# Optimization experiments

Measured on AMD Instinct MI355X. Metric: run time of the kernel, lower is better.

Reference implementation:

```python
import jax, jax.numpy as jnp
import numpy as np

B, S, HID, MEM, NW = 32, 256, 1024, 256, 1024
PLAST, IMP = 0.1, 1.0
W_SCALE = 0.02  # sane init for projection weights


def setup_inputs() -> dict:
    key = jax.random.key(0)
    ks = jax.random.split(key, 24)
    n = lambda k, sh, s=1.0: jax.random.normal(k, sh, dtype=jnp.float32) * s
    inp = {
        "q": n(ks[0], (B, S, HID)),
        "data": n(ks[1], (NW, HID)),
        "episodic_k": n(ks[2], (MEM, HID)),
        "episodic_v": n(ks[3], (MEM, HID)),
        "semantic_k": n(ks[4], (MEM, HID)),
        "semantic_v": n(ks[5], (MEM, HID)),
        "working_m": n(ks[6], (1, 10, HID)),
    }
    i = 7
    for name in ("atte", "atts", "attw"):
        inp[name + "_in_w"] = n(ks[i], (3 * HID, HID), W_SCALE); i += 1
        inp[name + "_in_b"] = jnp.zeros((3 * HID,), jnp.float32)
        inp[name + "_out_w"] = n(ks[i], (HID, HID), W_SCALE); i += 1
        inp[name + "_out_b"] = jnp.zeros((HID,), jnp.float32)
    inp["proj_w"] = n(ks[i], (HID, 3 * HID), W_SCALE)
    inp["proj_b"] = jnp.zeros((HID,), jnp.float32)
    return inp


def mha_shared_kv(q, k, v, in_w, in_b, out_w, out_b, n_heads):
    # q: [B,S,H]; k,v: [M,H] (memory bank shared across the batch)
    d = q.shape[-1] // n_heads
    wq, wk, wv = jnp.split(in_w, 3, axis=0)
    bq, bk, bv = jnp.split(in_b, 3)
    Bq, Sq, _ = q.shape
    M = k.shape[0]
    qh = (q @ wq.T + bq).reshape(Bq, Sq, n_heads, d)   # [B,S,h,d]
    kh = (k @ wk.T + bk).reshape(M, n_heads, d)        # [M,h,d]
    vh = (v @ wv.T + bv).reshape(M, n_heads, d)
    scale = 1.0 / jnp.sqrt(jnp.float32(d))
    att = jax.nn.softmax(jnp.einsum('bshd,mhd->bhsm', qh, kh) * scale, axis=-1)
    o = jnp.einsum('bhsm,mhd->bshd', att, vh).reshape(Bq, Sq, -1)
    return o @ out_w.T + out_b


def reference(q, data, episodic_k, episodic_v, semantic_k, semantic_v, working_m,
              atte_in_w, atte_in_b, atte_out_w, atte_out_b,
              atts_in_w, atts_in_b, atts_out_w, atts_out_b,
              attw_in_w, attw_in_b, attw_out_w, attw_out_b,
              proj_w, proj_b):
    # ---- write(data, 'episodic'): softmax-addressed fast-weight update ----
    probs = jax.nn.softmax(data @ episodic_k.T, axis=-1)          # [N,M]
    w = probs * (PLAST * IMP)                                     # [N,M]
    u = w.mean(axis=0)[:, None]                                   # [M,1] mean update strength per slot
    writes = jnp.einsum('nm,nh->mh', w, data) / NW                # mean_n data[n]*w[n,m]
    ek = jax.lax.stop_gradient(episodic_k * (1.0 - u) + writes)   # .data assignment -> no grad
    ev = jax.lax.stop_gradient(episodic_v * (1.0 - u) + writes)
    # ---- read(q): 3 small attentions over memory banks, concat, project ----
    e_r = mha_shared_kv(q, ek, ev, atte_in_w, atte_in_b, atte_out_w, atte_out_b, 16)
    s_r = mha_shared_kv(q, semantic_k, semantic_v, atts_in_w, atts_in_b, atts_out_w, atts_out_b, 16)
    w_r = mha_shared_kv(q, working_m[0], working_m[0], attw_in_w, attw_in_b, attw_out_w, attw_out_b, 8)
    cat = jnp.concatenate((e_r, s_r, w_r), axis=-1)               # [B,S,3H]
    return cat @ proj_w.T + proj_b                                # [B,S,H]
```

## Files before the change

### kernel.cpp

```cpp
#include <hip/hip_runtime.h>
#include <hip/hip_bf16.h>


using bf = __hip_bfloat16;
using short8v = __attribute__((ext_vector_type(8))) short;
using f32x4  = __attribute__((ext_vector_type(4))) float;

#define GLOAD_LDS16(g, l) __builtin_amdgcn_global_load_lds( \
    (const __attribute__((address_space(1))) void*)(g), \
    (__attribute__((address_space(3))) void*)(l), 16, 0, 0)

__device__ inline float bf2f(unsigned short s) {
    union { unsigned u; float f; } c; c.u = ((unsigned)s) << 16; return c.f;
}
__device__ inline unsigned short f2bu(float x) {
    union { float f; unsigned u; } c; c.f = x;
    unsigned r = c.u + 0x7FFF + ((c.u >> 16) & 1);
    return (unsigned short)(r >> 16);
}
__device__ inline void storeC(float* p, float v) { *p = v; }
__device__ inline void storeC(bf* p, float v) { *p = __float2bfloat16(v); }

__global__ __launch_bounds__(256) void gemm_bt(
    const bf* __restrict__ A, int lda,
    const bf* __restrict__ B, int ldb,
    float* __restrict__ part, int M, int N, int K)
{
    __shared__ short As[128 * 64];
    __shared__ short Bs[128 * 64];
    const int nbn = N >> 7;
    const int bm = blockIdx.x / nbn, bn = blockIdx.x % nbn;
    const int t = threadIdx.x;
    const int w = t >> 6, lane = t & 63;
    const int wr = w >> 1, wc = w & 1;
    const int l16 = lane & 15, lhi = lane >> 4;
    const int kc = K / gridDim.y;
    const int kbeg = blockIdx.y * kc, kend = kbeg + kc;

    f32x4 acc[4][4];
    #pragma unroll
    for (int i = 0; i < 4; ++i)
        #pragma unroll
        for (int j = 0; j < 4; ++j) { f32x4 z = {0.f, 0.f, 0.f, 0.f}; acc[i][j] = z; }

    const bf* Arow = A + (size_t)bm * 128 * lda;
    const bf* Brow = B + (size_t)bn * 128 * ldb;

    for (int k0 = kbeg; k0 < kend; k0 += 64) {
        #pragma unroll
        for (int j = 0; j < 4; ++j) {
            int u = (w * 4 + j) * 64 + lane;
            int row = u >> 3, c8 = u & 7;
            int slot = c8 ^ (row & 7);
            GLOAD_LDS16(Brow + (size_t)row * ldb + k0 + slot * 8, &Bs[(w * 4 + j) * 512]);
            GLOAD_LDS16(Arow + (size_t)row * lda + k0 + slot * 8, &As[(w * 4 + j) * 512]);
        }
        __syncthreads();
        #pragma unroll
        for (int kk = 0; kk < 2; ++kk) {
            short8v af[4], bfr[4];
            #pragma unroll
            for (int mt = 0; mt < 4; ++mt) {
                int row = wr * 64 + mt * 16 + l16;
                int slot = (kk * 4 + lhi) ^ (row & 7);
                af[mt] = *(const short8v*)&As[row * 64 + slot * 8];
            }
            #pragma unroll
            for (int nt = 0; nt < 4; ++nt) {
                int row = wc * 64 + nt * 16 + l16;
                int slot = (kk * 4 + lhi) ^ (row & 7);
                bfr[nt] = *(const short8v*)&Bs[row * 64 + slot * 8];
            }
            #pragma unroll
            for (int mt = 0; mt < 4; ++mt)
                #pragma unroll
                for (int nt = 0; nt < 4; ++nt)
                    acc[mt][nt] = __builtin_amdgcn_mfma_f32_16x16x32_bf16(
                        af[mt], bfr[nt], acc[mt][nt], 0, 0, 0);
        }
        __syncthreads();
    }
    #pragma unroll
    for (int mt = 0; mt < 4; ++mt)
        #pragma unroll
        for (int nt = 0; nt < 4; ++nt) {
            int col = bn * 128 + wc * 64 + nt * 16 + l16;
            #pragma unroll
            for (int j = 0; j < 4; ++j) {
                int rowg = bm * 128 + wr * 64 + mt * 16 + lhi * 4 + j;
                part[(size_t)blockIdx.y * M * N + (size_t)rowg * N + col] = acc[mt][nt][j];
            }
        }
}

template <typename CT>
__global__ __launch_bounds__(512) void gemm256(
    const bf* __restrict__ A, int lda,
    const bf* __restrict__ B, int ldb,
    const float* __restrict__ bias,
    CT* __restrict__ C, int ldc,
    int M, int N, int K)
{
    __shared__ short As[256 * 64];
    __shared__ short Bs[128 * 64];
    const int nbn = N >> 7;
    int bid = blockIdx.x;
    bid = (bid & 7) * (gridDim.x >> 3) + (bid >> 3);
    const int bm = bid / nbn, bn = bid % nbn;
    const int t = threadIdx.x;
    const int w = t >> 6, lane = t & 63;
    const int wr = w >> 1, wc = w & 1;
    const int l16 = lane & 15, lhi = lane >> 4;

    f32x4 acc[4][4];
    #pragma unroll
    for (int i = 0; i < 4; ++i)
        #pragma unroll
        for (int j = 0; j < 4; ++j) { f32x4 z = {0.f, 0.f, 0.f, 0.f}; acc[i][j] = z; }

    const bf* Arow = A + (size_t)bm * 256 * lda;
    const bf* Brow = B + (size_t)bn * 128 * ldb;

    for (int k0 = 0; k0 < K; k0 += 64) {
        #pragma unroll
        for (int j = 0; j < 2; ++j) {
            int u = t + (j << 9);
            int row = u >> 3, c8 = u & 7;
            int slot = c8 ^ (row & 7);
            GLOAD_LDS16(Brow + (size_t)row * ldb + k0 + slot * 8, &Bs[(j * 8 + w) * 512]);
        }
        #pragma unroll
        for (int j = 0; j < 4; ++j) {
            int u = t + (j << 9);
            int row = u >> 3, c8 = u & 7;
            int slot = c8 ^ (row & 7);
            GLOAD_LDS16(Arow + (size_t)row * lda + k0 + slot * 8, &As[(j * 8 + w) * 512]);
        }
        __syncthreads();
        #pragma unroll
        for (int kk = 0; kk < 2; ++kk) {
            short8v af[4], bfr[4];
            #pragma unroll
            for (int mt = 0; mt < 4; ++mt) {
                int row = wr * 64 + mt * 16 + l16;
                int slot = (kk * 4 + lhi) ^ (row & 7);
                af[mt] = *(const short8v*)&As[row * 64 + slot * 8];
            }
            #pragma unroll
            for (int nt = 0; nt < 4; ++nt) {
                int row = wc * 64 + nt * 16 + l16;
                int slot = (kk * 4 + lhi) ^ (row & 7);
                bfr[nt] = *(const short8v*)&Bs[row * 64 + slot * 8];
            }
            #pragma unroll
            for (int mt = 0; mt < 4; ++mt)
                #pragma unroll
                for (int nt = 0; nt < 4; ++nt)
                    acc[mt][nt] = __builtin_amdgcn_mfma_f32_16x16x32_bf16(
                        af[mt], bfr[nt], acc[mt][nt], 0, 0, 0);
        }
        __syncthreads();
    }
    #pragma unroll
    for (int mt = 0; mt < 4; ++mt)
        #pragma unroll
        for (int nt = 0; nt < 4; ++nt) {
            int col = bn * 128 + wc * 64 + nt * 16 + l16;
            float bv = bias ? bias[col] : 0.0f;
            #pragma unroll
            for (int j = 0; j < 4; ++j) {
                int rowg = bm * 256 + wr * 64 + mt * 16 + lhi * 4 + j;
                storeC(&C[(size_t)rowg * ldc + col], acc[mt][nt][j] + bv);
            }
        }
}

template <typename CT>
__global__ __launch_bounds__(512) void gemm256db(
    const bf* __restrict__ A, int lda,
    const bf* __restrict__ B, int ldb,
    const float* __restrict__ bias,
    CT* __restrict__ C, int ldc,
    int M, int N, int K)
{
    __shared__ short As0[256 * 64];
    __shared__ short Bs0[128 * 64];
    __shared__ short As1[256 * 64];
    __shared__ short Bs1[128 * 64];
    const int nbn = N >> 7;
    int bid = blockIdx.x;
    bid = (bid & 7) * (gridDim.x >> 3) + (bid >> 3);
    const int bm = bid / nbn, bn = bid % nbn;
    const int t = threadIdx.x;
    const int w = t >> 6, lane = t & 63;
    const int wr = w >> 1, wc = w & 1;
    const int l16 = lane & 15, lhi = lane >> 4;

    f32x4 acc[4][4];
    #pragma unroll
    for (int i = 0; i < 4; ++i)
        #pragma unroll
        for (int j = 0; j < 4; ++j) { f32x4 z = {0.f, 0.f, 0.f, 0.f}; acc[i][j] = z; }

    const bf* Arow = A + (size_t)bm * 256 * lda;
    const bf* Brow = B + (size_t)bn * 128 * ldb;

    auto stage = [&](short* Asd, short* Bsd, int k0) {
        #pragma unroll
        for (int j = 0; j < 2; ++j) {
            int u = t + (j << 9);
            int row = u >> 3, c8 = u & 7;
            int slot = c8 ^ (row & 7);
            GLOAD_LDS16(Brow + (size_t)row * ldb + k0 + slot * 8, &Bsd[(j * 8 + w) * 512]);
        }
        #pragma unroll
        for (int j = 0; j < 4; ++j) {
            int u = t + (j << 9);
            int row = u >> 3, c8 = u & 7;
            int slot = c8 ^ (row & 7);
            GLOAD_LDS16(Arow + (size_t)row * lda + k0 + slot * 8, &Asd[(j * 8 + w) * 512]);
        }
    };
    auto compute = [&](const short* Ass, const short* Bss) {
        #pragma unroll
        for (int kk = 0; kk < 2; ++kk) {
            short8v af[4], bfr[4];
            #pragma unroll
            for (int mt = 0; mt < 4; ++mt) {
                int row = wr * 64 + mt * 16 + l16;
                int slot = (kk * 4 + lhi) ^ (row & 7);
                af[mt] = *(const short8v*)&Ass[row * 64 + slot * 8];
            }
            #pragma unroll
            for (int nt = 0; nt < 4; ++nt) {
                int row = wc * 64 + nt * 16 + l16;
                int slot = (kk * 4 + lhi) ^ (row & 7);
                bfr[nt] = *(const short8v*)&Bss[row * 64 + slot * 8];
            }
            #pragma unroll
            for (int mt = 0; mt < 4; ++mt)
                #pragma unroll
                for (int nt = 0; nt < 4; ++nt)
                    acc[mt][nt] = __builtin_amdgcn_mfma_f32_16x16x32_bf16(
                        af[mt], bfr[nt], acc[mt][nt], 0, 0, 0);
        }
    };

    const int nt_ = K >> 6;
    stage(As0, Bs0, 0);
    stage(As1, Bs1, 64);
    asm volatile("s_waitcnt vmcnt(6)" ::: "memory");
    __builtin_amdgcn_sched_barrier(0);
    __builtin_amdgcn_s_barrier();

    for (int ti = 0; ti < nt_ - 2; ti += 2) {
        compute(As0, Bs0);
        __builtin_amdgcn_s_barrier();
        stage(As0, Bs0, (ti + 2) << 6);
        asm volatile("s_waitcnt vmcnt(6)" ::: "memory");
        __builtin_amdgcn_sched_barrier(0);
        __builtin_amdgcn_s_barrier();
        compute(As1, Bs1);
        __builtin_amdgcn_s_barrier();
        stage(As1, Bs1, (ti + 3) << 6);
        asm volatile("s_waitcnt vmcnt(6)" ::: "memory");
        __builtin_amdgcn_sched_barrier(0);
        __builtin_amdgcn_s_barrier();
    }
    compute(As0, Bs0);
    __builtin_amdgcn_s_barrier();
    asm volatile("s_waitcnt vmcnt(0)" ::: "memory");
    __builtin_amdgcn_sched_barrier(0);
    __builtin_amdgcn_s_barrier();
    compute(As1, Bs1);

    #pragma unroll
    for (int mt = 0; mt < 4; ++mt)
        #pragma unroll
        for (int nt = 0; nt < 4; ++nt) {
            int col = bn * 128 + wc * 64 + nt * 16 + l16;
            float bv = bias ? bias[col] : 0.0f;
            #pragma unroll
            for (int j = 0; j < 4; ++j) {
                int rowg = bm * 256 + wr * 64 + mt * 16 + lhi * 4 + j;
                storeC(&C[(size_t)rowg * ldc + col], acc[mt][nt][j] + bv);
            }
        }
}

struct GG { const bf* A; const bf* B; const float* bias; bf* out;
            int lda, ldb, M, N, ldo, xoff; };
struct GG7 { GG g[7]; };

__global__ __launch_bounds__(256) void ggemm(GG7 P)
{
    __shared__ short As[128 * 64];
    __shared__ short Bs[128 * 64];
    const int bid = blockIdx.x;
    int gidx = 0;
    #pragma unroll
    for (int i = 1; i < 7; ++i) if (bid >= P.g[i].xoff) gidx = i;
    const GG d = P.g[gidx];
    const int lb = bid - d.xoff;
    const int nbn = d.N >> 7;
    const int bm = lb / nbn, bn = lb % nbn;
    const int t = threadIdx.x;
    const int w = t >> 6, lane = t & 63;
    const int wr = w >> 1, wc = w & 1;
    const int l16 = lane & 15, lhi = lane >> 4;

    f32x4 acc[4][4];
    #pragma unroll
    for (int i = 0; i < 4; ++i)
        #pragma unroll
        for (int j = 0; j < 4; ++j) { f32x4 z = {0.f, 0.f, 0.f, 0.f}; acc[i][j] = z; }

    const bf* Afrow = d.A + (size_t)bm * 128 * d.lda;
    const bf* Brow  = d.B + (size_t)bn * 128 * d.ldb;

    for (int k0 = 0; k0 < 1024; k0 += 64) {
        #pragma unroll
        for (int j = 0; j < 4; ++j) {
            int u = (w * 4 + j) * 64 + lane;
            int row = u >> 3, c8 = u & 7;
            int slot = c8 ^ (row & 7);
            GLOAD_LDS16(Brow + (size_t)row * d.ldb + k0 + slot * 8, &Bs[(w * 4 + j) * 512]);
            GLOAD_LDS16(Afrow + (size_t)row * d.lda + k0 + slot * 8, &As[(w * 4 + j) * 512]);
        }
        __syncthreads();
        #pragma unroll
        for (int kk = 0; kk < 2; ++kk) {
            short8v af[4], bfr[4];
            #pragma unroll
            for (int mt = 0; mt < 4; ++mt) {
                int row = wr * 64 + mt * 16 + l16;
                int slot = (kk * 4 + lhi) ^ (row & 7);
                af[mt] = *(const short8v*)&As[row * 64 + slot * 8];
            }
            #pragma unroll
            for (int nt = 0; nt < 4; ++nt) {
                int row = wc * 64 + nt * 16 + l16;
                int slot = (kk * 4 + lhi) ^ (row & 7);
                bfr[nt] = *(const short8v*)&Bs[row * 64 + slot * 8];
            }
            #pragma unroll
            for (int mt = 0; mt < 4; ++mt)
                #pragma unroll
                for (int nt = 0; nt < 4; ++nt)
                    acc[mt][nt] = __builtin_amdgcn_mfma_f32_16x16x32_bf16(
                        af[mt], bfr[nt], acc[mt][nt], 0, 0, 0);
        }
        __syncthreads();
    }
    #pragma unroll
    for (int mt = 0; mt < 4; ++mt)
        #pragma unroll
        for (int nt = 0; nt < 4; ++nt) {
            int col = bn * 128 + wc * 64 + nt * 16 + l16;
            float bv = d.bias ? d.bias[col] : 0.0f;
            #pragma unroll
            for (int j = 0; j < 4; ++j) {
                int rowg = bm * 128 + wr * 64 + mt * 16 + lhi * 4 + j;
                d.out[(size_t)rowg * d.ldo + col]
                    = __float2bfloat16(acc[mt][nt][j] + bv);
            }
        }
}

__global__ __launch_bounds__(512) void attn_es(
    bf* Ocat, const bf* __restrict__ khE, const bf* __restrict__ khS,
    const bf* __restrict__ vTE, const bf* __restrict__ vTS)
{
    __shared__ short Ks[256 * 64];
    __shared__ short Vs[64 * 256];
    const int bank = blockIdx.x >> 10;
    const int lbid = blockIdx.x & 1023;
    const bf* kh  = bank ? khS : khE;
    const bf* vhT = bank ? vTS : vTE;
    bf* QO = Ocat + bank * 1024;
    const int qt = lbid >> 4, head = lbid & 15;
    const int t = threadIdx.x, w = t >> 6, lane = t & 63;
    const int l16 = lane & 15, lhi = lane >> 4;
    const float scale = 0.125f;

    #pragma unroll
    for (int j = 0; j < 4; ++j) {
        int ublk = w * 4 + j;
        int u = ublk * 64 + lane;
        { int row = u >> 3, c8 = u & 7;
          int slot = c8 ^ (row & 7);
          GLOAD_LDS16(kh + (size_t)row * 1024 + head * 64 + slot * 8, &Ks[ublk * 512]); }
        { int row = u >> 5, c16 = u & 31;
          int slot = c16 ^ (row & 7);
          GLOAD_LDS16(vhT + (size_t)(head * 64 + row) * 256 + slot * 8, &Vs[ublk * 512]); }
    }
    const int qr = qt * 128 + w * 16 + l16;
    short8v aq0 = *(const short8v*)(QO + (size_t)qr * 3072 + head * 64 + lhi * 8);
    short8v aq1 = *(const short8v*)(QO + (size_t)qr * 3072 + head * 64 + 32 + lhi * 8);
    __syncthreads();

    f32x4 sc[16];
    #pragma unroll
    for (int nt = 0; nt < 16; ++nt) { f32x4 z = {0.f, 0.f, 0.f, 0.f}; sc[nt] = z; }
    #pragma unroll
    for (int nt = 0; nt < 16; ++nt) {
        int row = nt * 16 + l16;
        #pragma unroll
        for (int kk = 0; kk < 2; ++kk) {
            int slot = (kk * 4 + lhi) ^ (row & 7);
            short8v b = *(const short8v*)&Ks[row * 64 + slot * 8];
            sc[nt] = __builtin_amdgcn_mfma_f32_16x16x32_bf16(kk ? aq1 : aq0, b, sc[nt], 0, 0, 0);
        }
    }
    float inv[4];
    #pragma unroll
    for (int j = 0; j < 4; ++j) {
        float m_ = -1e30f;
        #pragma unroll
        for (int nt = 0; nt < 16; ++nt) m_ = fmaxf(m_, sc[nt][j]);
        #pragma unroll
        for (int off = 8; off; off >>= 1) m_ = fmaxf(m_, __shfl_xor(m_, off));
        float s_ = 0.f;
        #pragma unroll
        for (int nt = 0; nt < 16; ++nt) {
            float e = __expf((sc[nt][j] - m_) * scale);
            sc[nt][j] = e; s_ += e;
        }
        #pragma unroll
        for (int off = 8; off; off >>= 1) s_ += __shfl_xor(s_, off);
        inv[j] = 1.0f / s_;
    }
    __syncthreads();

    char* Pw = (char*)Ks + w * 4096;
    f32x4 oa[4];
    #pragma unroll
    for (int nt = 0; nt < 4; ++nt) { f32x4 z = {0.f, 0.f, 0.f, 0.f}; oa[nt] = z; }
    #pragma unroll
    for (int h = 0; h < 2; ++h) {
        #pragma unroll
        for (int nt = 0; nt < 8; ++nt) {
            int colL = nt * 16 + l16;
            #pragma unroll
            for (int j = 0; j < 4; ++j) {
                int row = lhi * 4 + j;
                *(short*)(Pw + row * 256 + ((colL * 2) ^ ((row & 7) << 4)))
                    = (short)f2bu(sc[h * 8 + nt][j] * inv[j]);
            }
        }
        #pragma unroll
        for (int kk = 0; kk < 4; ++kk) {
            short8v a = *(const short8v*)(Pw + l16 * 256 + (((kk * 32 + lhi * 8) * 2) ^ ((l16 & 7) << 4)));
            #pragma unroll
            for (int nt = 0; nt < 4; ++nt) {
                int row = nt * 16 + l16;
                int m = h * 128 + kk * 32 + lhi * 8;
                short8v b = *(const short8v*)((const char*)Vs + row * 512 + ((m * 2) ^ ((row & 7) << 4)));
                oa[nt] = __builtin_amdgcn_mfma_f32_16x16x32_bf16(a, b, oa[nt], 0, 0, 0);
            }
        }
    }
    #pragma unroll
    for (int nt = 0; nt < 4; ++nt)
        #pragma unroll
        for (int j = 0; j < 4; ++j)
            QO[(size_t)(qt * 128 + w * 16 + lhi * 4 + j) * 3072 + head * 64 + nt * 16 + l16]
                = __float2bfloat16(oa[nt][j]);
}

__global__ __launch_bounds__(256) void attn_w(
    bf* QOp, const bf* __restrict__ khw, const bf* __restrict__ vhw)
{
    const int t = threadIdx.x;
    const int head = t >> 5;
    const int dg = head * 128 + (t & 31) * 4;

    ushort4 kv[10], vv[10];
    #pragma unroll
    for (int m = 0; m < 10; ++m) {
        kv[m] = *(const ushort4*)(khw + (size_t)m * 1024 + dg);
        vv[m] = *(const ushort4*)(vhw + (size_t)m * 1024 + dg);
    }
    #pragma unroll
    for (int r = 0; r < 4; ++r) {
        const int bs = blockIdx.x * 4 + r;
        ushort4 qv = *(const ushort4*)(QOp + (size_t)bs * 3072 + dg);
        float q0 = bf2f(qv.x), q1 = bf2f(qv.y), q2 = bf2f(qv.z), q3 = bf2f(qv.w);
        float s[10];
        #pragma unroll
        for (int m = 0; m < 10; ++m) {
            float pr = q0 * bf2f(kv[m].x) + q1 * bf2f(kv[m].y)
                     + q2 * bf2f(kv[m].z) + q3 * bf2f(kv[m].w);
            #pragma unroll
            for (int off = 16; off; off >>= 1) pr += __shfl_xor(pr, off);
            s[m] = pr * 0.08838834764831845f;
        }
        float mx = s[0];
        #pragma unroll
        for (int m = 1; m < 10; ++m) mx = fmaxf(mx, s[m]);
        float pp[10], sum = 0.f;
        #pragma unroll
        for (int m = 0; m < 10; ++m) { pp[m] = __expf(s[m] - mx); sum += pp[m]; }
        float inv = 1.0f / sum;
        float o0 = 0, o1 = 0, o2 = 0, o3 = 0;
        #pragma unroll
        for (int m = 0; m < 10; ++m) {
            o0 += pp[m] * bf2f(vv[m].x); o1 += pp[m] * bf2f(vv[m].y);
            o2 += pp[m] * bf2f(vv[m].z); o3 += pp[m] * bf2f(vv[m].w);
        }
        bf* op = QOp + (size_t)bs * 3072 + dg;
        op[0] = __float2bfloat16(o0 * inv); op[1] = __float2bfloat16(o1 * inv);
        op[2] = __float2bfloat16(o2 * inv); op[3] = __float2bfloat16(o3 * inv);
    }
}

struct CS { const float* src; bf* dst; int voff; };
struct MP {
    CS cs[13];
    const float* tsrc[4]; bf* tdst[4];
    const float* ow[3]; const float* ob[3]; const float* ib[3];
    float* bp;
    const float* inb_e; const float* inb_s; float* bqcat3;
    const float* wm; const float* inw_w; const float* inb_w;
    bf* khw; bf* vhw;
};

__global__ __launch_bounds__(256) void megaprep(MP P)
{
    __shared__ unsigned short tile[64][65];
    const int bid = blockIdx.x;
    const int t = threadIdx.x;
    if (bid < 20224) {
        int gi = bid * 256 + t;
        int gidx = 0;
        #pragma unroll
        for (int i = 1; i < 13; ++i) if (gi >= P.cs[i].voff) gidx = i;
        int i = (gi - P.cs[gidx].voff) * 4;
        float4 v = *(const float4*)(P.cs[gidx].src + i);
        ushort4 o;
        o.x = f2bu(v.x); o.y = f2bu(v.y); o.z = f2bu(v.z); o.w = f2bu(v.w);
        *(ushort4*)((unsigned short*)P.cs[gidx].dst + i) = o;
    } else if (bid < 21248) {
        int lb = bid - 20224;
        int sel = lb >> 8, bb = lb & 255;
        const float* in = P.tsrc[sel];
        bf* outT = P.tdst[sel];
        int bx = bb & 15, by = bb >> 4;
        int r0 = by * 64, c0 = bx * 64;
        int tr = t >> 4, tc4 = (t & 15) * 4;
        #pragma unroll
        for (int i = 0; i < 4; ++i) {
            int r = tr + i * 16;
            float4 v = *(const float4*)(in + (size_t)(r0 + r) * 1024 + c0 + tc4);
            tile[r][tc4 + 0] = f2bu(v.x); tile[r][tc4 + 1] = f2bu(v.y);
            tile[r][tc4 + 2] = f2bu(v.z); tile[r][tc4 + 3] = f2bu(v.w);
        }
        __syncthreads();
        #pragma unroll
        for (int i = 0; i < 4; ++i) {
            int r = tr + i * 16;
            ushort4 v;
            v.x = tile[tc4 + 0][r]; v.y = tile[tc4 + 1][r];
            v.z = tile[tc4 + 2][r]; v.w = tile[tc4 + 3][r];
            *(ushort4*)((unsigned short*)outT + (size_t)(c0 + r) * 1024 + r0 + tc4) = v;
        }
    } else if (bid < 22016) {
        int g = (bid - 21248) * 4 + (t >> 6);
        int lane = t & 63;
        int bank = g >> 10, j = g & 1023;
        const float* ow = P.ow[bank];
        const float* xx = P.ib[bank] + 2048;
        const float* wrow = ow + (size_t)j * 1024;
        float acc = 0.f;
        #pragma unroll
        for (int cc = 0; cc < 4; ++cc) {
            float4 a = *(const float4*)(wrow + lane * 16 + cc * 4);
            float4 x = *(const float4*)(xx + lane * 16 + cc * 4);
            acc += a.x * x.x + a.y * x.y + a.z * x.z + a.w * x.w;
        }
        #pragma unroll
        for (int off = 32; off; off >>= 1) acc += __shfl_xor(acc, off);
        if (lane == 0) P.bp[g] = acc + P.ob[bank][j];
    } else if (bid < 22028) {
        int i = (bid - 22016) * 256 + t;
        if (i < 1024) P.bqcat3[i] = P.inb_e[i];
        else if (i < 2048) P.bqcat3[i] = P.inb_s[i - 1024];
        else P.bqcat3[i] = P.inb_w[i - 2048];
    } else {
        int o = (bid - 22028) * 4 + (t >> 6);
        int lane = t & 63;
        int sel = o >= 10240;
        int o2 = o - sel * 10240;
        int m = o2 >> 10, c = o2 & 1023;
        const float* wrow = P.inw_w + (size_t)(1024 + sel * 1024 + c) * 1024;
        const float* xrow = P.wm + (size_t)m * 1024;
        float acc = 0.f;
        #pragma unroll
        for (int cc = 0; cc < 4; ++cc) {
            float4 a = *(const float4*)(wrow + lane * 16 + cc * 4);
            float4 x = *(const float4*)(xrow + lane * 16 + cc * 4);
            acc += a.x * x.x + a.y * x.y + a.z * x.z + a.w * x.w;
        }
        #pragma unroll
        for (int off = 32; off; off >>= 1) acc += __shfl_xor(acc, off);
        if (lane == 0) {
            float v = acc + (sel ? 0.f : P.inb_w[1024 + c]);
            (sel ? P.vhw : P.khw)[(size_t)m * 1024 + c] = __float2bfloat16(v);
        }
    }
}


__global__ __launch_bounds__(256) void btot_kern(
    const float* __restrict__ bp, const float* __restrict__ pw,
    const float* __restrict__ pb, float* __restrict__ btot)
{
    int j = blockIdx.x * 4 + (threadIdx.x >> 6);
    int lane = threadIdx.x & 63;
    const float* row = pw + (size_t)j * 3072;
    float acc = 0.f;
    #pragma unroll
    for (int it = 0; it < 12; ++it) {
        int c = lane * 4 + it * 256;
        float4 a = *(const float4*)(row + c);
        float4 x = *(const float4*)(bp + c);
        acc += a.x * x.x + a.y * x.y + a.z * x.z + a.w * x.w;
    }
    #pragma unroll
    for (int off = 32; off; off >>= 1) acc += __shfl_xor(acc, off);
    if (lane == 0) btot[j] = acc + pb[j];
}

__global__ __launch_bounds__(256) void write_softmax_p(const float* __restrict__ part,
                                                       bf* __restrict__ wT)
{
    const int n = blockIdx.x, m = threadIdx.x;
    float s = 0.f;
    #pragma unroll
    for (int k = 0; k < 8; ++k) s += part[(size_t)k * 262144 + n * 256 + m];
    float mx = s;
    #pragma unroll
    for (int off = 32; off; off >>= 1) mx = fmaxf(mx, __shfl_xor(mx, off));
    __shared__ float red[4], red2[4];
    int w = threadIdx.x >> 6;
    if ((threadIdx.x & 63) == 0) red[w] = mx;
    __syncthreads();
    mx = fmaxf(fmaxf(red[0], red[1]), fmaxf(red[2], red[3]));
    float e = __expf(s - mx);
    float sm = e;
    #pragma unroll
    for (int off = 32; off; off >>= 1) sm += __shfl_xor(sm, off);
    if ((threadIdx.x & 63) == 0) red2[w] = sm;
    __syncthreads();
    sm = red2[0] + red2[1] + red2[2] + red2[3];
    wT[(size_t)m * 1024 + n] = __float2bfloat16(0.1f * e / sm);
}

__global__ __launch_bounds__(256) void update_fused(
    const float* __restrict__ epk, const float* __restrict__ epv,
    const bf* __restrict__ wT, const float* __restrict__ part,
    bf* __restrict__ ekb, bf* __restrict__ evb)
{
    __shared__ float red[4];
    const int m = blockIdx.x, t = threadIdx.x;
    ushort4 wv = *(const ushort4*)((const unsigned short*)wT + (size_t)m * 1024 + t * 4);
    float s = bf2f(wv.x) + bf2f(wv.y) + bf2f(wv.z) + bf2f(wv.w);
    #pragma unroll
    for (int off = 32; off; off >>= 1) s += __shfl_xor(s, off);
    if ((t & 63) == 0) red[t >> 6] = s;
    __syncthreads();
    float f = 1.0f - (red[0] + red[1] + red[2] + red[3]) * (1.0f / 1024.0f);
    int base = m * 1024 + t * 4;
    float4 wr = *(const float4*)(part + base);
    #pragma unroll
    for (int k = 1; k < 8; ++k) {
        float4 v = *(const float4*)(part + (size_t)k * 262144 + base);
        wr.x += v.x; wr.y += v.y; wr.z += v.z; wr.w += v.w;
    }
    const float sc = 1.0f / 1024.0f;
    float4 pk = *(const float4*)(epk + base);
    float4 pv = *(const float4*)(epv + base);
    ushort4 ok, ov;
    ok.x = f2bu(pk.x * f + wr.x * sc); ok.y = f2bu(pk.y * f + wr.y * sc);
    ok.z = f2bu(pk.z * f + wr.z * sc); ok.w = f2bu(pk.w * f + wr.w * sc);
    ov.x = f2bu(pv.x * f + wr.x * sc); ov.y = f2bu(pv.y * f + wr.y * sc);
    ov.z = f2bu(pv.z * f + wr.z * sc); ov.w = f2bu(pv.w * f + wr.w * sc);
    *(ushort4*)((unsigned short*)ekb + base) = ok;
    *(ushort4*)((unsigned short*)evb + base) = ov;
}

extern "C" void kernel_launch(void* const* d_in, const int* in_sizes, int n_in,
                              void* d_out, int out_size, void* d_ws, size_t ws_size,
                              hipStream_t stream)
{
    const float* q     = (const float*)d_in[0];
    const float* data  = (const float*)d_in[1];
    const float* epk   = (const float*)d_in[2];
    const float* epv   = (const float*)d_in[3];
    const float* smk   = (const float*)d_in[4];
    const float* smv   = (const float*)d_in[5];
    const float* wm    = (const float*)d_in[6];
    const float* inw_e = (const float*)d_in[7];  const float* inb_e = (const float*)d_in[8];
    const float* ow_e  = (const float*)d_in[9];  const float* ob_e  = (const float*)d_in[10];
    const float* inw_s = (const float*)d_in[11]; const float* inb_s = (const float*)d_in[12];
    const float* ow_s  = (const float*)d_in[13]; const float* ob_s  = (const float*)d_in[14];
    const float* inw_w = (const float*)d_in[15]; const float* inb_w = (const float*)d_in[16];
    const float* ow_w  = (const float*)d_in[17]; const float* ob_w  = (const float*)d_in[18];
    const float* pw    = (const float*)d_in[19]; const float* pb    = (const float*)d_in[20];
    float* out  = (float*)d_out;
    float* part = (float*)d_out;
    bf* qb  = (bf*)((char*)d_out + 8388608);
    bf* pwb = (bf*)((char*)d_out + 25165824);

    char* p = (char*)d_ws;
    auto alloc = [&](size_t bytes) -> char* {
        char* r = p; p += (bytes + 255) & ~(size_t)255; return r;
    };
    float* bp     = (float*)alloc(3072 * 4);
    float* btot   = (float*)alloc(1024 * 4);
    float* bqcat3 = (float*)alloc(3072 * 4);
    bf* wT     = (bf*)alloc(256 * 1024 * 2);
    bf* dT     = (bf*)alloc((size_t)1024 * 1024 * 2);
    bf* datab  = (bf*)alloc((size_t)1024 * 1024 * 2);
    bf* epkb   = (bf*)alloc(256 * 1024 * 2);
    bf* smkb   = (bf*)alloc(256 * 1024 * 2);
    bf* smvb   = (bf*)alloc(256 * 1024 * 2);
    bf* ekb    = (bf*)alloc(256 * 1024 * 2);
    bf* evb    = (bf*)alloc(256 * 1024 * 2);
    bf* khE    = (bf*)alloc(256 * 1024 * 2);
    bf* khS    = (bf*)alloc(256 * 1024 * 2);
    bf* vTE    = (bf*)alloc((size_t)1024 * 256 * 2);
    bf* vTS    = (bf*)alloc((size_t)1024 * 256 * 2);
    bf* khw    = (bf*)alloc(10 * 1024 * 2);
    bf* vhw    = (bf*)alloc(10 * 1024 * 2);
    bf* Wall   = (bf*)alloc((size_t)3072 * 1024 * 2);
    bf* WkE    = (bf*)alloc((size_t)1024 * 1024 * 2);
    bf* WkS    = (bf*)alloc((size_t)1024 * 1024 * 2);
    bf* WvE    = (bf*)alloc((size_t)1024 * 1024 * 2);
    bf* WvS    = (bf*)alloc((size_t)1024 * 1024 * 2);
    bf* owT0   = (bf*)alloc((size_t)1024 * 1024 * 2);
    bf* owT1   = (bf*)alloc((size_t)1024 * 1024 * 2);
    bf* owT2   = (bf*)alloc((size_t)1024 * 1024 * 2);
    bf* Gcat   = (bf*)alloc((size_t)1024 * 3072 * 2);
    bf* Ocat   = (bf*)alloc((size_t)8192 * 3072 * 2);
    if ((size_t)(p - (char*)d_ws) > ws_size) return;

    {
        MP P;
        CS cs[13] = { {q, qb, 0},
                      {epk,  epkb, 2097152}, {smv, smvb, 2162688},
                      {inw_e, Wall, 2228224},
                      {inw_s, Wall + (size_t)1024 * 1024, 2490368},
                      {inw_w, Wall + (size_t)2048 * 1024, 2752512},
                      {inw_e + (size_t)1024 * 1024, WkE, 3014656},
                      {inw_s + (size_t)1024 * 1024, WkS, 3276800},
                      {data, datab, 3538944},
                      {pw, pwb, 3801088},
                      {smk, smkb, 4587520},
                      {inw_e + (size_t)2048 * 1024, WvE, 4653056},
                      {inw_s + (size_t)2048 * 1024, WvS, 4915200} };
        for (int i = 0; i < 13; ++i) P.cs[i] = cs[i];
        P.tsrc[0] = data; P.tdst[0] = dT;
        P.tsrc[1] = ow_e; P.tdst[1] = owT0;
        P.tsrc[2] = ow_s; P.tdst[2] = owT1;
        P.tsrc[3] = ow_w; P.tdst[3] = owT2;
        P.ow[0] = ow_e; P.ow[1] = ow_s; P.ow[2] = ow_w;
        P.ob[0] = ob_e; P.ob[1] = ob_s; P.ob[2] = ob_w;
        P.ib[0] = inb_e; P.ib[1] = inb_s; P.ib[2] = inb_w;
        P.bp = bp;
        P.inb_e = inb_e; P.inb_s = inb_s; P.bqcat3 = bqcat3;
        P.wm = wm; P.inw_w = inw_w; P.inb_w = inb_w;
        P.khw = khw; P.vhw = vhw;
        megaprep<<<27148, 256, 0, stream>>>(P);
    }
    btot_kern<<<256, 256, 0, stream>>>(bp, pw, pb, btot);

    gemm_bt<<<dim3(16, 8), 256, 0, stream>>>(datab, 1024, epkb, 1024, part, 1024, 256, 1024);
    write_softmax_p<<<1024, 256, 0, stream>>>(part, wT);
    gemm_bt<<<dim3(16, 8), 256, 0, stream>>>(wT, 1024, dT, 1024, part, 256, 1024, 1024);
    update_fused<<<256, 256, 0, stream>>>(epk, epv, wT, part, ekb, evb);

    gemm256<bf><<<768, 512, 0, stream>>>(
        qb, 1024, Wall, 1024, bqcat3, Ocat, 3072, 8192, 3072, 1024);

    {
        GG7 G = {{
            { ekb,        WkE,  inb_e + 1024, khE,         1024, 1024,  256, 1024, 1024, 0   },
            { smkb,       WkS,  inb_s + 1024, khS,         1024, 1024,  256, 1024, 1024, 16  },
            { WvE,        evb,  nullptr,      vTE,         1024, 1024, 1024,  256,  256, 32  },
            { WvS,        smvb, nullptr,      vTS,         1024, 1024, 1024,  256,  256, 48  },
            { pwb + 0,    owT0, nullptr,      Gcat + 0,    3072, 1024, 1024, 1024, 3072, 64  },
            { pwb + 1024, owT1, nullptr,      Gcat + 1024, 3072, 1024, 1024, 1024, 3072, 128 },
            { pwb + 2048, owT2, nullptr,      Gcat + 2048, 3072, 1024, 1024, 1024, 3072, 192 },
        }};
        ggemm<<<256, 256, 0, stream>>>(G);
    }

    attn_es<<<2048, 512, 0, stream>>>(Ocat, khE, khS, vTE, vTS);
    attn_w<<<2048, 256, 0, stream>>>(Ocat + 2048, khw, vhw);

    gemm256db<float><<<256, 512, 0, stream>>>(
        Ocat, 3072, Gcat, 3072, btot, out, 1024, 8192, 1024, 3072);
}
```

Baseline: 266.4 us.

## Double-buffer LDS tiles in grouped GEMM to overlap loads with MFMA

The grouped bf16 GEMM kernel now uses two LDS buffers for A and B and prefetches the next K-tile with global_load_lds while computing on the current one. Partial vmcnt waits and raw s_barriers replace the per-iteration full __syncthreads pairs. The aim is to hide global-memory latency behind MFMA work, at the cost of doubling LDS use to 64KB per block, which may lower occupancy. The hand-written waitcnt counts assume exactly 8 outstanding loads per stage.

```diff
diff --git a/kernel.cpp b/kernel.cpp
--- a/kernel.cpp
+++ b/kernel.cpp
@@ -294,8 +294,10 @@
 
 __global__ __launch_bounds__(256) void ggemm(GG7 P)
 {
-    __shared__ short As[128 * 64];
-    __shared__ short Bs[128 * 64];
+    __shared__ short As0[128 * 64];
+    __shared__ short Bs0[128 * 64];
+    __shared__ short As1[128 * 64];
+    __shared__ short Bs1[128 * 64];
     const int bid = blockIdx.x;
     int gidx = 0;
     #pragma unroll
@@ -318,16 +320,17 @@
     const bf* Afrow = d.A + (size_t)bm * 128 * d.lda;
     const bf* Brow  = d.B + (size_t)bn * 128 * d.ldb;
 
-    for (int k0 = 0; k0 < 1024; k0 += 64) {
+    auto stage = [&](short* Asd, short* Bsd, int k0) {
         #pragma unroll
         for (int j = 0; j < 4; ++j) {
             int u = (w * 4 + j) * 64 + lane;
             int row = u >> 3, c8 = u & 7;
             int slot = c8 ^ (row & 7);
-            GLOAD_LDS16(Brow + (size_t)row * d.ldb + k0 + slot * 8, &Bs[(w * 4 + j) * 512]);
-            GLOAD_LDS16(Afrow + (size_t)row * d.lda + k0 + slot * 8, &As[(w * 4 + j) * 512]);
-        }
-        __syncthreads();
+            GLOAD_LDS16(Brow + (size_t)row * d.ldb + k0 + slot * 8, &Bsd[(w * 4 + j) * 512]);
+            GLOAD_LDS16(Afrow + (size_t)row * d.lda + k0 + slot * 8, &Asd[(w * 4 + j) * 512]);
+        }
+    };
+    auto compute = [&](const short* Ass, const short* Bss) {
         #pragma unroll
         for (int kk = 0; kk < 2; ++kk) {
             short8v af[4], bfr[4];
@@ -335,13 +338,13 @@
             for (int mt = 0; mt < 4; ++mt) {
                 int row = wr * 64 + mt * 16 + l16;
                 int slot = (kk * 4 + lhi) ^ (row & 7);
-                af[mt] = *(const short8v*)&As[row * 64 + slot * 8];
+                af[mt] = *(const short8v*)&Ass[row * 64 + slot * 8];
             }
             #pragma unroll
             for (int nt = 0; nt < 4; ++nt) {
                 int row = wc * 64 + nt * 16 + l16;
                 int slot = (kk * 4 + lhi) ^ (row & 7);
-                bfr[nt] = *(const short8v*)&Bs[row * 64 + slot * 8];
+                bfr[nt] = *(const short8v*)&Bss[row * 64 + slot * 8];
             }
             #pragma unroll
             for (int mt = 0; mt < 4; ++mt)
@@ -350,8 +353,35 @@
                     acc[mt][nt] = __builtin_amdgcn_mfma_f32_16x16x32_bf16(
                         af[mt], bfr[nt], acc[mt][nt], 0, 0, 0);
         }
-        __syncthreads();
-    }
+    };
+
+    stage(As0, Bs0, 0);
+    stage(As1, Bs1, 64);
+    asm volatile("s_waitcnt vmcnt(8)" ::: "memory");
+    __builtin_amdgcn_sched_barrier(0);
+    __builtin_amdgcn_s_barrier();
+
+    for (int ti = 0; ti < 14; ti += 2) {
+        compute(As0, Bs0);
+        __builtin_amdgcn_s_barrier();
+        stage(As0, Bs0, (ti + 2) << 6);
+        asm volatile("s_waitcnt vmcnt(8)" ::: "memory");
+        __builtin_amdgcn_sched_barrier(0);
+        __builtin_amdgcn_s_barrier();
+        compute(As1, Bs1);
+        __builtin_amdgcn_s_barrier();
+        stage(As1, Bs1, (ti + 3) << 6);
+        asm volatile("s_waitcnt vmcnt(8)" ::: "memory");
+        __builtin_amdgcn_sched_barrier(0);
+        __builtin_amdgcn_s_barrier();
+    }
+    compute(As0, Bs0);
+    __builtin_amdgcn_s_barrier();
+    asm volatile("s_waitcnt vmcnt(0)" ::: "memory");
+    __builtin_amdgcn_sched_barrier(0);
+    __builtin_amdgcn_s_barrier();
+    compute(As1, Bs1);
+
     #pragma unroll
     for (int mt = 0; mt < 4; ++mt)
         #pragma unroll
```

Result: no change. 262.9 us, median of 2 (-1.3%).
